# Kernel tuning notes

Hardware: AMD Instinct MI355X
Metric: run time of the kernel (lower is better)

## Reference

```python
import jax, jax.numpy as jnp
import numpy as np

B, T, D, H = 4, 2048, 1024, 16
HD = D // H  # 64


def setup_inputs() -> dict:
    key = jax.random.key(0)
    ks = jax.random.split(key, 5)
    return {
        "x": jax.random.normal(ks[0], (B, T, D), dtype=jnp.float32),
        "W_qkv": jax.random.normal(ks[1], (D, 3 * D), dtype=jnp.float32) * 0.02,
        "b_qkv": jax.random.normal(ks[2], (3 * D,), dtype=jnp.float32) * 0.02,
        "W_out": jax.random.normal(ks[3], (D, D), dtype=jnp.float32) * 0.02,
        "b_out": jax.random.normal(ks[4], (D,), dtype=jnp.float32) * 0.02,
        "mask": 1,
    }


def reference(x, W_qkv, b_qkv, W_out, b_out, mask):
    # fused QKV projection: (B,T,3D)
    qkv = x @ W_qkv + b_qkv
    # torch layout: view (B,T,H,3*hd) then chunk last dim into q,k,v
    qkv = qkv.reshape(B, T, H, 3, HD)
    q = qkv[..., 0, :].transpose(0, 2, 1, 3)  # (B,H,T,hd)
    k = qkv[..., 1, :].transpose(0, 2, 1, 3)
    v = qkv[..., 2, :].transpose(0, 2, 1, 3)
    scores = jnp.einsum('bhqd,bhkd->bhqk', q, k) / jnp.sqrt(jnp.float32(HD))
    if mask:
        causal = jnp.triu(jnp.ones((T, T), dtype=bool), k=1)
        scores = jnp.where(causal[None, None], jnp.float32(-jnp.inf), scores)
    attn = jax.nn.softmax(scores, axis=-1)
    out = jnp.einsum('bhqk,bhkd->bhqd', attn, v)  # (B,H,T,hd)
    out = out.transpose(0, 2, 1, 3).reshape(B, T, D)
    return out @ W_out + b_out
```

## Files before the change

### kernel.cpp

```cpp
#include <hip/hip_runtime.h>

typedef unsigned short u16;
typedef __bf16 bf16x8 __attribute__((ext_vector_type(8)));
typedef float f32x4 __attribute__((ext_vector_type(4)));
typedef float f32x16 __attribute__((ext_vector_type(16)));

#define DEV __device__ __forceinline__

constexpr int Bb = 4, Tt = 2048, Dd = 1024, Hh = 16, HDd = 64;
constexpr int MM = Bb * Tt;
constexpr float QSCALE = 0.125f * 1.4426950408889634f;

DEV u16 f2bf(float f) {
  unsigned u = __float_as_uint(f);
  u += 0x7fffu + ((u >> 16) & 1u);
  return (u16)(u >> 16);
}

DEV unsigned cvtpk(float a, float b) {
  unsigned r;
  asm("v_cvt_pk_bf16_f32 %0, %1, %2" : "=v"(r) : "v"(a), "v"(b));
  return r;
}

DEV void pswap(unsigned& a, unsigned& b) {
  asm("v_permlane32_swap_b32 %0, %1" : "+v"(a), "+v"(b));
}

DEV void gload_lds16(const u16* g, u16* l) {
  __builtin_amdgcn_global_load_lds(
      (const __attribute__((address_space(1))) void*)g,
      (__attribute__((address_space(3))) void*)l, 16, 0, 0);
}

__global__ __launch_bounds__(256) void cast_x_kernel(const float* __restrict__ in,
                                                     u16* __restrict__ out, int n8) {
  int i = blockIdx.x * 256 + threadIdx.x;
  if (i >= n8) return;
  const float4* p = (const float4*)in + (size_t)i * 2;
  float4 v0 = p[0], v1 = p[1];
  union { u16 u[8]; uint4 v; } t;
  t.u[0] = f2bf(v0.x); t.u[1] = f2bf(v0.y); t.u[2] = f2bf(v0.z); t.u[3] = f2bf(v0.w);
  t.u[4] = f2bf(v1.x); t.u[5] = f2bf(v1.y); t.u[6] = f2bf(v1.z); t.u[7] = f2bf(v1.w);
  ((uint4*)out)[i] = t.v;
}

__global__ __launch_bounds__(256) void wcast_t_kernel(const float* __restrict__ in,
                                                      u16* __restrict__ out, int K, int N) {
  __shared__ float tile[32][33];
  int n0 = blockIdx.x * 32, k0 = blockIdx.y * 32;
  int tx = threadIdx.x & 31, ty = threadIdx.x >> 5;
  #pragma unroll
  for (int yy = ty; yy < 32; yy += 8)
    tile[yy][tx] = in[(size_t)(k0 + yy) * N + n0 + tx];
  __syncthreads();
  #pragma unroll
  for (int yy = ty; yy < 32; yy += 8)
    out[(size_t)(n0 + yy) * K + k0 + tx] = f2bf(tile[tx][yy]);
}

__global__ __launch_bounds__(256) void vtrans_kernel(const u16* __restrict__ V,
                                                     u16* __restrict__ Vt) {
  __shared__ u16 tile[32][33];
  size_t base = (size_t)blockIdx.z * Tt * HDd;
  int t0 = blockIdx.x * 32, d0 = blockIdx.y * 32;
  int tx = threadIdx.x & 31, ty = threadIdx.x >> 5;
  #pragma unroll
  for (int yy = ty; yy < 32; yy += 8)
    tile[yy][tx] = V[base + (size_t)(t0 + yy) * HDd + d0 + tx];
  __syncthreads();
  #pragma unroll
  for (int yy = ty; yy < 32; yy += 8)
    Vt[base + (size_t)(d0 + yy) * Tt + t0 + tx] = tile[tx][yy];
}

DEV void stage_tile(const u16* __restrict__ src, int row0, int k0, int ld, u16* lds) {
  int t = threadIdx.x, w = t >> 6;
  #pragma unroll
  for (int j = 0; j < 2; ++j) {
    int e = (j * 256 + t) * 8;
    int r = e >> 5;
    int slot = (e >> 3) & 3;
    int c = (slot ^ ((r >> 1) & 3)) << 3;
    gload_lds16(src + (size_t)(row0 + r) * ld + k0 + c, lds + j * 2048 + w * 512);
  }
}

template <int EPI>
__global__ __launch_bounds__(256) void gemm_bt_kernel(
    const u16* __restrict__ A, const u16* __restrict__ Bt,
    const float* __restrict__ bias, float* __restrict__ Cf,
    u16* __restrict__ Qb, u16* __restrict__ Kb, u16* __restrict__ Vb,
    int M, int N, int Kd) {
  __shared__ __align__(16) u16 SH[16384];
  int nx = N >> 7;
  int bid = blockIdx.y * nx + blockIdx.x;
  int nwg = (M >> 7) * nx;
  int swz = (bid & 7) * (nwg >> 3) + (bid >> 3);
  int m0 = (swz / nx) * 128, n0 = (swz % nx) * 128;

  int tid = threadIdx.x, l = tid & 63, w = tid >> 6;
  int lo = l & 15, g = l >> 4;
  int wm = (w >> 1) * 64, wn = (w & 1) * 64;
  f32x4 acc[4][4] = {};
  stage_tile(A, m0, 0, Kd, SH);
  stage_tile(Bt, n0, 0, Kd, SH + 8192);
  __syncthreads();
  int nk = Kd >> 5;
  for (int kt = 0; kt < nk; ++kt) {
    int cur = kt & 1;
    if (kt + 1 < nk) {
      stage_tile(A, m0, (kt + 1) * 32, Kd, SH + (cur ^ 1) * 4096);
      stage_tile(Bt, n0, (kt + 1) * 32, Kd, SH + 8192 + (cur ^ 1) * 4096);
    }
    const u16* Ac = SH + cur * 4096;
    const u16* Bc = SH + 8192 + cur * 4096;
    bf16x8 a[4], b[4];
    #pragma unroll
    for (int i = 0; i < 4; ++i) {
      int row = wm + i * 16 + lo;
      a[i] = *(const bf16x8*)&Ac[row * 32 + ((g ^ ((row >> 1) & 3)) << 3)];
    }
    #pragma unroll
    for (int j = 0; j < 4; ++j) {
      int row = wn + j * 16 + lo;
      b[j] = *(const bf16x8*)&Bc[row * 32 + ((g ^ ((row >> 1) & 3)) << 3)];
    }
    #pragma unroll
    for (int i = 0; i < 4; ++i)
      #pragma unroll
      for (int j = 0; j < 4; ++j)
        acc[i][j] = __builtin_amdgcn_mfma_f32_16x16x32_bf16(a[i], b[j], acc[i][j], 0, 0, 0);
    __syncthreads();
  }
  if (EPI == 0) {
    u16* ep = SH + w * 4096;
    int nblk = n0 + wn;
    int hh = nblk / 192, which = (nblk % 192) >> 6;
    float qs = (which == 0) ? QSCALE : 1.0f;
    #pragma unroll
    for (int j = 0; j < 4; ++j) {
      float bv = bias[nblk + j * 16 + lo];
      int slot = j * 2 + (lo >> 3);
      #pragma unroll
      for (int i = 0; i < 4; ++i) {
        #pragma unroll
        for (int r = 0; r < 4; ++r) {
          int lrow = i * 16 + g * 4 + r;
          ep[lrow * 64 + ((slot ^ (lrow & 7)) << 3) + (lo & 7)] =
              f2bf((acc[i][j][r] + bv) * qs);
        }
      }
    }
    asm volatile("s_waitcnt lgkmcnt(0)" ::: "memory");
    u16* dst = (which == 0) ? Qb : (which == 1) ? Kb : Vb;
    int mblk = m0 + wm;
    int b_ = mblk >> 11, t0 = mblk & (Tt - 1);
    dst += ((size_t)(b_ * Hh + hh) * Tt + t0) * HDd;
    #pragma unroll
    for (int s = 0; s < 8; ++s) {
      int row = s * 8 + (l >> 3);
      int phys = ((l & 7) ^ (row & 7)) << 3;
      uint4 v = *(const uint4*)&ep[row * 64 + phys];
      *(uint4*)(dst + row * 64 + (l & 7) * 8) = v;
    }
  } else {
    #pragma unroll
    for (int j = 0; j < 4; ++j) {
      int n = n0 + wn + j * 16 + lo;
      float bv = bias[n];
      #pragma unroll
      for (int i = 0; i < 4; ++i) {
        #pragma unroll
        for (int r = 0; r < 4; ++r) {
          int m = m0 + wm + i * 16 + g * 4 + r;
          Cf[(size_t)m * N + n] = acc[i][j][r] + bv;
        }
      }
    }
  }
}

DEV void stage64x64(const u16* __restrict__ g, size_t rstride, u16* lds) {
  int t = threadIdx.x, w = t >> 6;
  #pragma unroll
  for (int j = 0; j < 2; ++j) {
    int e = j * 256 + t;
    int r = e >> 3, p = e & 7;
    int lg = p ^ (r & 7);
    gload_lds16(g + (size_t)r * rstride + lg * 8, lds + (size_t)(j * 256 + w * 64) * 8);
  }
}

DEV void build_pfrags(const f32x16& s, bf16x8& f0, bf16x8& f1) {
  unsigned w0 = cvtpk(s[0], s[1]),  w1 = cvtpk(s[2], s[3]);
  unsigned w2 = cvtpk(s[4], s[5]),  w3 = cvtpk(s[6], s[7]);
  unsigned w4 = cvtpk(s[8], s[9]),  w5 = cvtpk(s[10], s[11]);
  unsigned w6 = cvtpk(s[12], s[13]), w7 = cvtpk(s[14], s[15]);
  pswap(w0, w2);
  pswap(w1, w3);
  pswap(w4, w6);
  pswap(w5, w7);
  union { unsigned u[4]; bf16x8 v; } t0, t1;
  t0.u[0] = w0; t0.u[1] = w1; t0.u[2] = w2; t0.u[3] = w3;
  t1.u[0] = w4; t1.u[1] = w5; t1.u[2] = w6; t1.u[3] = w7;
  f0 = t0.v; f1 = t1.v;
}

DEV void write_o(u16* __restrict__ O, size_t rowbase, const f32x16& o0,
                 const f32x16& o1, float L, int hf) {
  float inv = 1.0f / L;
  #pragma unroll
  for (int m = 0; m < 4; ++m) {
    uint2 v0, v1;
    v0.x = cvtpk(o0[4 * m] * inv,     o0[4 * m + 1] * inv);
    v0.y = cvtpk(o0[4 * m + 2] * inv, o0[4 * m + 3] * inv);
    *(uint2*)(O + rowbase + m * 8 + hf * 4) = v0;
    v1.x = cvtpk(o1[4 * m] * inv,     o1[4 * m + 1] * inv);
    v1.y = cvtpk(o1[4 * m + 2] * inv, o1[4 * m + 3] * inv);
    *(uint2*)(O + rowbase + 32 + m * 8 + hf * 4) = v1;
  }
}

__global__ __launch_bounds__(256) void attn_kernel(const u16* __restrict__ Q,
                                                   const u16* __restrict__ K,
                                                   const u16* __restrict__ Vt,
                                                   u16* __restrict__ O) {
  __shared__ __align__(16) u16 Ks[3][4096];
  __shared__ __align__(16) u16 Vs[3][4096];
  int p = blockIdx.y & 7;
  int bh = ((int)blockIdx.y >> 3) * 8 + (int)blockIdx.x;
  int b_ = bh >> 4, h = bh & 15;
  const u16* Qp = Q + (size_t)bh * Tt * HDd;
  const u16* Kp = K + (size_t)bh * Tt * HDd;
  const u16* Vp = Vt + (size_t)bh * HDd * Tt;
  int tid = threadIdx.x, w = tid >> 6, l = tid & 63;
  int lq = l & 31, hf = l >> 5;
  int JA = 15 - p, JB = p;
  int ntA = 2 * JA + 2, ntB = 2 * JB + 2, ntT = ntA + ntB;

  int q0 = 128 * JA + 32 * w;
  int qrow = q0 + lq;

  bf16x8 aq[4];
  #pragma unroll
  for (int s = 0; s < 4; ++s)
    aq[s] = *(const bf16x8*)(Qp + (size_t)qrow * HDd + s * 16 + hf * 8);

  f32x16 o0 = {}, o1 = {};
  float M = -1e30f, L = 0.f;

  stage64x64(Kp, HDd, Ks[0]);
  stage64x64(Vp, Tt, Vs[0]);
  stage64x64(Kp + (size_t)64 * HDd, HDd, Ks[1]);
  stage64x64(Vp + 64, Tt, Vs[1]);
  asm volatile("s_waitcnt vmcnt(4)" ::: "memory");
  __builtin_amdgcn_s_barrier();

  for (int it = 0; it < ntT; ++it) {
    if (it == ntA) {
      size_t rbA = ((size_t)b_ * Tt + qrow) * Dd + h * HDd;
      write_o(O, rbA, o0, o1, L, hf);
      #pragma unroll
      for (int r = 0; r < 16; ++r) { o0[r] = 0.f; o1[r] = 0.f; }
      M = -1e30f; L = 0.f;
      q0 = 128 * JB + 32 * w;
      qrow = q0 + lq;
      #pragma unroll
      for (int s = 0; s < 4; ++s)
        aq[s] = *(const bf16x8*)(Qp + (size_t)qrow * HDd + s * 16 + hf * 8);
    }
    if (it + 2 < ntT) {
      int t2 = it + 2;
      int nkt = (t2 < ntA ? t2 : t2 - ntA) * 64;
      int bi = t2 % 3;
      stage64x64(Kp + (size_t)nkt * HDd, HDd, Ks[bi]);
      stage64x64(Vp + nkt, Tt, Vs[bi]);
    }
    int kt = (it < ntA ? it : it - ntA) * 64;
    const u16* Kc = Ks[it % 3];
    const u16* Vc = Vs[it % 3];
    if (kt < q0 + 32) {
      f32x16 s0 = {}, s1 = {};
      int swz = lq & 7;
      __builtin_amdgcn_s_setprio(1);
      #pragma unroll
      for (int ds = 0; ds < 4; ++ds) {
        int slot = 2 * ds + hf;
        bf16x8 k0 = *(const bf16x8*)&Kc[lq * 64 + ((slot ^ swz) << 3)];
        bf16x8 k1 = *(const bf16x8*)&Kc[(32 + lq) * 64 + ((slot ^ swz) << 3)];
        s0 = __builtin_amdgcn_mfma_f32_32x32x16_bf16(k0, aq[ds], s0, 0, 0, 0);
        s1 = __builtin_amdgcn_mfma_f32_32x32x16_bf16(k1, aq[ds], s1, 0, 0, 0);
      }
      __builtin_amdgcn_s_setprio(0);
      if (kt + 63 > q0) {
        #pragma unroll
        for (int r = 0; r < 16; ++r) {
          int kg = kt + (r & 3) + 8 * (r >> 2) + 4 * hf;
          if (kg > qrow)      s0[r] = -INFINITY;
          if (kg + 32 > qrow) s1[r] = -INFINITY;
        }
      }
      float mx_[16];
      #pragma unroll
      for (int r = 0; r < 16; ++r) mx_[r] = fmaxf(s0[r], s1[r]);
      #pragma unroll
      for (int st = 8; st >= 1; st >>= 1)
        #pragma unroll
        for (int r = 0; r < 16; ++r) if (r < st) mx_[r] = fmaxf(mx_[r], mx_[r + st]);
      float mx = fmaxf(mx_[0], __shfl_xor(mx_[0], 32));
      float sc = 1.f;
      if (!__all(mx <= M + 8.f)) {
        float Mn = fmaxf(M, mx);
        sc = __builtin_amdgcn_exp2f(M - Mn);
        M = Mn;
        #pragma unroll
        for (int r = 0; r < 16; ++r) { o0[r] *= sc; o1[r] *= sc; }
      }
      #pragma unroll
      for (int r = 0; r < 16; ++r) {
        s0[r] = __builtin_amdgcn_exp2f(s0[r] - M);
        s1[r] = __builtin_amdgcn_exp2f(s1[r] - M);
      }
      float ls_[16];
      #pragma unroll
      for (int r = 0; r < 16; ++r) ls_[r] = s0[r] + s1[r];
      #pragma unroll
      for (int st = 8; st >= 1; st >>= 1)
        #pragma unroll
        for (int r = 0; r < 16; ++r) if (r < st) ls_[r] += ls_[r + st];
      float ls = ls_[0] + __shfl_xor(ls_[0], 32);
      L = L * sc + ls;
      bf16x8 pf0, pf1, pf2, pf3;
      build_pfrags(s0, pf0, pf1);
      build_pfrags(s1, pf2, pf3);
      __builtin_amdgcn_s_setprio(1);
      #pragma unroll
      for (int ks = 0; ks < 4; ++ks) {
        int slot = 2 * ks + hf;
        bf16x8 v0 = *(const bf16x8*)&Vc[lq * 64 + ((slot ^ swz) << 3)];
        bf16x8 v1 = *(const bf16x8*)&Vc[(32 + lq) * 64 + ((slot ^ swz) << 3)];
        bf16x8 pf = (ks == 0) ? pf0 : (ks == 1) ? pf1 : (ks == 2) ? pf2 : pf3;
        o0 = __builtin_amdgcn_mfma_f32_32x32x16_bf16(v0, pf, o0, 0, 0, 0);
        o1 = __builtin_amdgcn_mfma_f32_32x32x16_bf16(v1, pf, o1, 0, 0, 0);
      }
      __builtin_amdgcn_s_setprio(0);
    }
    if (it + 2 < ntT) {
      asm volatile("s_waitcnt vmcnt(4)" ::: "memory");
    } else {
      asm volatile("s_waitcnt vmcnt(0)" ::: "memory");
    }
    __builtin_amdgcn_s_barrier();
  }

  size_t rbB = ((size_t)b_ * Tt + qrow) * Dd + h * HDd;
  write_o(O, rbB, o0, o1, L, hf);
}

extern "C" void kernel_launch(void* const* d_in, const int* in_sizes, int n_in,
                              void* d_out, int out_size, void* d_ws, size_t ws_size,
                              hipStream_t stream) {
  const float* x    = (const float*)d_in[0];
  const float* Wqkv = (const float*)d_in[1];
  const float* bqkv = (const float*)d_in[2];
  const float* Wout = (const float*)d_in[3];
  const float* bout = (const float*)d_in[4];
  float* out = (float*)d_out;
  char* ws = (char*)d_ws;

  u16* xb    = (u16*)(ws + 0);
  u16* Wqkvt = (u16*)(ws + 16777216);
  u16* Woutt = (u16*)(ws + 23068672);
  u16* Qb    = (u16*)(ws + 25165824);
  u16* Kb    = (u16*)(ws + 41943040);
  u16* Vb    = (u16*)(ws + 58720256);
  u16* Vtb   = (u16*)(ws + 0);
  u16* Ob    = (u16*)(ws + 58720256);

  cast_x_kernel<<<4096, 256, 0, stream>>>(x, xb, (MM * Dd) / 8);
  wcast_t_kernel<<<dim3(96, 32), 256, 0, stream>>>(Wqkv, Wqkvt, Dd, 3 * Dd);
  wcast_t_kernel<<<dim3(32, 32), 256, 0, stream>>>(Wout, Woutt, Dd, Dd);
  gemm_bt_kernel<0><<<dim3(24, 64), 256, 0, stream>>>(
      xb, Wqkvt, bqkv, nullptr, Qb, Kb, Vb, MM, 3 * Dd, Dd);
  vtrans_kernel<<<dim3(Tt / 32, HDd / 32, Bb * Hh), 256, 0, stream>>>(Vb, Vtb);
  attn_kernel<<<dim3(8, 64), 256, 0, stream>>>(Qb, Kb, Vtb, Ob);
  gemm_bt_kernel<1><<<dim3(8, 64), 256, 0, stream>>>(
      Ob, Woutt, bout, out, nullptr, nullptr, nullptr, MM, Dd, Dd);
}
```

Measured before the change: 188.4 us.

## Triple-buffer GEMM K-loop and fuse V transpose into QKV epilogue

The GEMM main loop moves from double to triple buffering in LDS, prefetching two K-tiles ahead and using explicit vmcnt waits with raw barriers in place of __syncthreads. The QKV epilogue now writes V directly in transposed (HD x T) layout through a swizzled LDS tile, so the separate vtrans kernel launch and its extra global round trip are removed. LDS use per block rises from 32 KB to 48 KB, which may lower occupancy. The workspace layout is rearranged so Ob aliases xb.

```diff
diff --git a/kernel.cpp b/kernel.cpp
--- a/kernel.cpp
+++ b/kernel.cpp
@@ -59,21 +59,6 @@
     out[(size_t)(n0 + yy) * K + k0 + tx] = f2bf(tile[tx][yy]);
 }
 
-__global__ __launch_bounds__(256) void vtrans_kernel(const u16* __restrict__ V,
-                                                     u16* __restrict__ Vt) {
-  __shared__ u16 tile[32][33];
-  size_t base = (size_t)blockIdx.z * Tt * HDd;
-  int t0 = blockIdx.x * 32, d0 = blockIdx.y * 32;
-  int tx = threadIdx.x & 31, ty = threadIdx.x >> 5;
-  #pragma unroll
-  for (int yy = ty; yy < 32; yy += 8)
-    tile[yy][tx] = V[base + (size_t)(t0 + yy) * HDd + d0 + tx];
-  __syncthreads();
-  #pragma unroll
-  for (int yy = ty; yy < 32; yy += 8)
-    Vt[base + (size_t)(d0 + yy) * Tt + t0 + tx] = tile[tx][yy];
-}
-
 DEV void stage_tile(const u16* __restrict__ src, int row0, int k0, int ld, u16* lds) {
   int t = threadIdx.x, w = t >> 6;
   #pragma unroll
@@ -90,9 +75,9 @@
 __global__ __launch_bounds__(256) void gemm_bt_kernel(
     const u16* __restrict__ A, const u16* __restrict__ Bt,
     const float* __restrict__ bias, float* __restrict__ Cf,
-    u16* __restrict__ Qb, u16* __restrict__ Kb, u16* __restrict__ Vb,
+    u16* __restrict__ Qb, u16* __restrict__ Kb, u16* __restrict__ Vtb,
     int M, int N, int Kd) {
-  __shared__ __align__(16) u16 SH[16384];
+  __shared__ __align__(16) u16 SH[24576];
   int nx = N >> 7;
   int bid = blockIdx.y * nx + blockIdx.x;
   int nwg = (M >> 7) * nx;
@@ -103,18 +88,21 @@
   int lo = l & 15, g = l >> 4;
   int wm = (w >> 1) * 64, wn = (w & 1) * 64;
   f32x4 acc[4][4] = {};
+  int nk = Kd >> 5;
   stage_tile(A, m0, 0, Kd, SH);
-  stage_tile(Bt, n0, 0, Kd, SH + 8192);
-  __syncthreads();
-  int nk = Kd >> 5;
+  stage_tile(Bt, n0, 0, Kd, SH + 12288);
+  stage_tile(A, m0, 32, Kd, SH + 4096);
+  stage_tile(Bt, n0, 32, Kd, SH + 12288 + 4096);
+  asm volatile("s_waitcnt vmcnt(4)" ::: "memory");
+  __builtin_amdgcn_s_barrier();
   for (int kt = 0; kt < nk; ++kt) {
-    int cur = kt & 1;
-    if (kt + 1 < nk) {
-      stage_tile(A, m0, (kt + 1) * 32, Kd, SH + (cur ^ 1) * 4096);
-      stage_tile(Bt, n0, (kt + 1) * 32, Kd, SH + 8192 + (cur ^ 1) * 4096);
-    }
-    const u16* Ac = SH + cur * 4096;
-    const u16* Bc = SH + 8192 + cur * 4096;
+    if (kt + 2 < nk) {
+      int bi = (kt + 2) % 3;
+      stage_tile(A, m0, (kt + 2) * 32, Kd, SH + bi * 4096);
+      stage_tile(Bt, n0, (kt + 2) * 32, Kd, SH + 12288 + bi * 4096);
+    }
+    const u16* Ac = SH + (kt % 3) * 4096;
+    const u16* Bc = SH + 12288 + (kt % 3) * 4096;
     bf16x8 a[4], b[4];
     #pragma unroll
     for (int i = 0; i < 4; ++i) {
@@ -131,38 +119,69 @@
       #pragma unroll
       for (int j = 0; j < 4; ++j)
         acc[i][j] = __builtin_amdgcn_mfma_f32_16x16x32_bf16(a[i], b[j], acc[i][j], 0, 0, 0);
-    __syncthreads();
+    if (kt + 2 < nk) {
+      asm volatile("s_waitcnt vmcnt(4)" ::: "memory");
+    } else {
+      asm volatile("s_waitcnt vmcnt(0)" ::: "memory");
+    }
+    __builtin_amdgcn_s_barrier();
   }
   if (EPI == 0) {
     u16* ep = SH + w * 4096;
     int nblk = n0 + wn;
     int hh = nblk / 192, which = (nblk % 192) >> 6;
-    float qs = (which == 0) ? QSCALE : 1.0f;
-    #pragma unroll
-    for (int j = 0; j < 4; ++j) {
-      float bv = bias[nblk + j * 16 + lo];
-      int slot = j * 2 + (lo >> 3);
-      #pragma unroll
-      for (int i = 0; i < 4; ++i) {
-        #pragma unroll
-        for (int r = 0; r < 4; ++r) {
-          int lrow = i * 16 + g * 4 + r;
-          ep[lrow * 64 + ((slot ^ (lrow & 7)) << 3) + (lo & 7)] =
-              f2bf((acc[i][j][r] + bv) * qs);
-        }
-      }
-    }
-    asm volatile("s_waitcnt lgkmcnt(0)" ::: "memory");
-    u16* dst = (which == 0) ? Qb : (which == 1) ? Kb : Vb;
     int mblk = m0 + wm;
     int b_ = mblk >> 11, t0 = mblk & (Tt - 1);
-    dst += ((size_t)(b_ * Hh + hh) * Tt + t0) * HDd;
-    #pragma unroll
-    for (int s = 0; s < 8; ++s) {
-      int row = s * 8 + (l >> 3);
-      int phys = ((l & 7) ^ (row & 7)) << 3;
-      uint4 v = *(const uint4*)&ep[row * 64 + phys];
-      *(uint4*)(dst + row * 64 + (l & 7) * 8) = v;
+    if (which == 2) {
+      #pragma unroll
+      for (int j = 0; j < 4; ++j) {
+        float bv = bias[nblk + j * 16 + lo];
+        int rowp = j * 16 + lo;
+        #pragma unroll
+        for (int i = 0; i < 4; ++i) {
+          int slotp = i * 2 + (g >> 1);
+          #pragma unroll
+          for (int r = 0; r < 4; ++r) {
+            ep[rowp * 64 + ((slotp ^ (rowp & 7)) << 3) + (g & 1) * 4 + r] =
+                f2bf(acc[i][j][r] + bv);
+          }
+        }
+      }
+      asm volatile("s_waitcnt lgkmcnt(0)" ::: "memory");
+      u16* dst = Vtb + (size_t)(b_ * Hh + hh) * HDd * Tt + t0;
+      #pragma unroll
+      for (int s = 0; s < 8; ++s) {
+        int row = s * 8 + (l >> 3);
+        int phys = ((l & 7) ^ (row & 7)) << 3;
+        uint4 v = *(const uint4*)&ep[row * 64 + phys];
+        *(uint4*)(dst + (size_t)row * Tt + (l & 7) * 8) = v;
+      }
+    } else {
+      float qs = (which == 0) ? QSCALE : 1.0f;
+      #pragma unroll
+      for (int j = 0; j < 4; ++j) {
+        float bv = bias[nblk + j * 16 + lo];
+        int slot = j * 2 + (lo >> 3);
+        #pragma unroll
+        for (int i = 0; i < 4; ++i) {
+          #pragma unroll
+          for (int r = 0; r < 4; ++r) {
+            int lrow = i * 16 + g * 4 + r;
+            ep[lrow * 64 + ((slot ^ (lrow & 7)) << 3) + (lo & 7)] =
+                f2bf((acc[i][j][r] + bv) * qs);
+          }
+        }
+      }
+      asm volatile("s_waitcnt lgkmcnt(0)" ::: "memory");
+      u16* dst = (which == 0) ? Qb : Kb;
+      dst += ((size_t)(b_ * Hh + hh) * Tt + t0) * HDd;
+      #pragma unroll
+      for (int s = 0; s < 8; ++s) {
+        int row = s * 8 + (l >> 3);
+        int phys = ((l & 7) ^ (row & 7)) << 3;
+        uint4 v = *(const uint4*)&ep[row * 64 + phys];
+        *(uint4*)(dst + row * 64 + (l & 7) * 8) = v;
+      }
     }
   } else {
     #pragma unroll
@@ -370,20 +389,18 @@
   char* ws = (char*)d_ws;
 
   u16* xb    = (u16*)(ws + 0);
+  u16* Ob    = (u16*)(ws + 0);
   u16* Wqkvt = (u16*)(ws + 16777216);
   u16* Woutt = (u16*)(ws + 23068672);
   u16* Qb    = (u16*)(ws + 25165824);
   u16* Kb    = (u16*)(ws + 41943040);
-  u16* Vb    = (u16*)(ws + 58720256);
-  u16* Vtb   = (u16*)(ws + 0);
-  u16* Ob    = (u16*)(ws + 58720256);
+  u16* Vtb   = (u16*)(ws + 58720256);
 
   cast_x_kernel<<<4096, 256, 0, stream>>>(x, xb, (MM * Dd) / 8);
   wcast_t_kernel<<<dim3(96, 32), 256, 0, stream>>>(Wqkv, Wqkvt, Dd, 3 * Dd);
   wcast_t_kernel<<<dim3(32, 32), 256, 0, stream>>>(Wout, Woutt, Dd, Dd);
   gemm_bt_kernel<0><<<dim3(24, 64), 256, 0, stream>>>(
-      xb, Wqkvt, bqkv, nullptr, Qb, Kb, Vb, MM, 3 * Dd, Dd);
-  vtrans_kernel<<<dim3(Tt / 32, HDd / 32, Bb * Hh), 256, 0, stream>>>(Vb, Vtb);
+      xb, Wqkvt, bqkv, nullptr, Qb, Kb, Vtb, MM, 3 * Dd, Dd);
   attn_kernel<<<dim3(8, 64), 256, 0, stream>>>(Qb, Kb, Vtb, Ob);
   gemm_bt_kernel<1><<<dim3(8, 64), 256, 0, stream>>>(
       Ob, Woutt, bout, out, nullptr, nullptr, nullptr, MM, Dd, Dd);
```

Measured after the change: 180.1 us. 1.05x faster.
